# Kernel optimization log

Hardware: AMD Instinct MI355X
Metric: run time of the kernel (lower is better)

The kernel has to match this reference:

```python
import jax, jax.numpy as jnp
import numpy as np

L, B, E, H = 2048, 2, 1024, 16
HD = E // H


def setup_inputs() -> dict:
    key = jax.random.key(0)
    ks = jax.random.split(key, 5)
    s = 0.02
    return {
        "query": jax.random.normal(ks[0], (L, B, E), jnp.float32),
        "key": jax.random.normal(ks[1], (L, B, E), jnp.float32),
        "value": jax.random.normal(ks[2], (L, B, E), jnp.float32),
        "in_proj_weight": jax.random.normal(ks[3], (3 * E, E), jnp.float32) * s,
        "in_proj_bias": jnp.zeros((3 * E,), jnp.float32),
        "out_proj_weight": jax.random.normal(ks[4], (E, E), jnp.float32) * s,
        "out_proj_bias": jnp.zeros((E,), jnp.float32),
    }


def reference(query, key, value, in_proj_weight, in_proj_bias, out_proj_weight, out_proj_bias):
    # torch nn.MultiheadAttention math, seq-first [L, B, E], causal mask
    # (attend_mode='only_attend_front': positions j > i are masked).
    w_q, w_k, w_v = jnp.split(in_proj_weight, 3, axis=0)
    b_q, b_k, b_v = jnpp_split(in_proj_bias) if False else jnp.split(in_proj_bias, 3, axis=0)
    q = query @ w_q.T + b_q            # [L, B, E]
    k = key @ w_k.T + b_k
    v = value @ w_v.T + b_v

    def heads(x):  # [L, B, E] -> [B, H, L, HD]
        return x.reshape(x.shape[0], x.shape[1], H, HD).transpose(1, 2, 0, 3)

    qh, kh, vh = heads(q), heads(k), heads(v)
    scale = 1.0 / jnp.sqrt(jnp.asarray(HD, q.dtype))
    scores = jnp.einsum("bhqd,bhkd->bhqk", qh * scale, kh)  # [B, H, L, L]
    causal = jnp.triu(jnp.ones((scores.shape[-2], scores.shape[-1]), bool), k=1)
    scores = jnp.where(causal, jnp.asarray(-jnp.inf, scores.dtype), scores)
    attn = jax.nn.softmax(scores, axis=-1)
    out = jnp.einsum("bhqk,bhkd->bhqd", attn, vh)           # [B, H, L, HD]
    out = out.transpose(2, 0, 1, 3).reshape(query.shape[0], query.shape[1], E)  # [L, B, E]
    out = out @ out_proj_weight.T + out_proj_bias
    # torch also returns head-averaged attn weights [B, L, L]
    attn_avg = attn.mean(axis=1)
    return out, attn_avg
```

## Files before the change

### kernel.cpp

```cpp
#include <hip/hip_runtime.h>

#define L_ 2048
#define B_ 2
#define E_ 1024
#define H_ 16
#define HD_ 64
#define M_ 4096
#define K_ 1024

typedef unsigned short u16;
typedef unsigned int u32;
using short8  = __attribute__((ext_vector_type(8))) short;
using short4v = __attribute__((ext_vector_type(4))) short;
using floatx4 = __attribute__((ext_vector_type(4))) float;

__device__ inline u16 f2b(float f) {
  unsigned u = __float_as_uint(f);
  u += 0x7FFF + ((u >> 16) & 1);
  return (u16)(u >> 16);
}

__device__ inline u32 pack2(float a, float b) {
  u32 ua = __float_as_uint(a) + 0x8000u;
  u32 ub = __float_as_uint(b) + 0x8000u;
  return (ua >> 16) | (ub & 0xFFFF0000u);
}

__device__ inline floatx4 mfma16(short8 a, short8 b, floatx4 c) {
  return __builtin_amdgcn_mfma_f32_16x16x32_bf16(a, b, c, 0, 0, 0);
}

__device__ inline void gload16(const void* g, void* l) {
  __builtin_amdgcn_global_load_lds(
      (const __attribute__((address_space(1))) u32*)g,
      (__attribute__((address_space(3))) u32*)l, 16, 0, 0);
}

__global__ void convk(const float* __restrict__ src, u16* __restrict__ dst, int n4) {
  int i = blockIdx.x * blockDim.x + threadIdx.x;
  if (i < n4) {
    float4 v = ((const float4*)src)[i];
    ushort4 o;
    o.x = f2b(v.x); o.y = f2b(v.y); o.z = f2b(v.z); o.w = f2b(v.w);
    ((ushort4*)dst)[i] = o;
  }
}

template <int MODE>
__global__ __launch_bounds__(256) void gemm128(
    const u16* __restrict__ A, const u16* __restrict__ W, const float* __restrict__ bias,
    u16* __restrict__ qh, u16* __restrict__ kh, u16* __restrict__ vhT,
    float* __restrict__ outp)
{
  __shared__ __align__(16) u16 As[128 * 32];
  __shared__ __align__(16) u16 Bs[128 * 32];
  const int p = (MODE == 0) ? blockIdx.z : 0;
  const u16* Ap = A + (size_t)p * M_ * K_;
  const u16* Wp = W + (size_t)p * E_ * K_;
  const float* bp = bias + p * E_;
  const int row0 = blockIdx.y * 128, col0 = blockIdx.x * 128;
  const int t = threadIdx.x, lane = t & 63, wv = t >> 6;
  const int lanem = lane & 15, quad = lane >> 4;
  const int wm = wv >> 1, wn = wv & 1;

  int f0 = t, f1 = 256 + t;
  int r0s = f0 >> 2, q0s = (f0 & 3) ^ ((r0s >> 1) & 3);
  int r1s = f1 >> 2, q1s = (f1 & 3) ^ ((r1s >> 1) & 3);

  floatx4 acc[4][4];
#pragma unroll
  for (int mi = 0; mi < 4; ++mi)
#pragma unroll
    for (int ni = 0; ni < 4; ++ni) acc[mi][ni] = (floatx4){0.f, 0.f, 0.f, 0.f};

  const int swz = (lanem >> 1) & 3;

  for (int k0 = 0; k0 < K_; k0 += 32) {
    __syncthreads();
    gload16(Ap + (size_t)(row0 + r0s) * K_ + k0 + q0s * 8, (char*)As + wv * 1024);
    gload16(Wp + (size_t)(col0 + r0s) * K_ + k0 + q0s * 8, (char*)Bs + wv * 1024);
    gload16(Ap + (size_t)(row0 + r1s) * K_ + k0 + q1s * 8, (char*)As + 4096 + wv * 1024);
    gload16(Wp + (size_t)(col0 + r1s) * K_ + k0 + q1s * 8, (char*)Bs + 4096 + wv * 1024);
    __syncthreads();
    short8 af[4], bfg[4];
#pragma unroll
    for (int mi = 0; mi < 4; ++mi) {
      int r = wm * 64 + mi * 16 + lanem;
      af[mi] = *(const short8*)((const char*)As + r * 64 + (quad ^ swz) * 16);
    }
#pragma unroll
    for (int ni = 0; ni < 4; ++ni) {
      int r = wn * 64 + ni * 16 + lanem;
      bfg[ni] = *(const short8*)((const char*)Bs + r * 64 + (quad ^ swz) * 16);
    }
#pragma unroll
    for (int mi = 0; mi < 4; ++mi)
#pragma unroll
      for (int ni = 0; ni < 4; ++ni)
        acc[mi][ni] = mfma16(af[mi], bfg[ni], acc[mi][ni]);
  }

#pragma unroll
  for (int ni = 0; ni < 4; ++ni) {
    int gc = col0 + wn * 64 + ni * 16 + lanem;
    float bv = bp[gc];
#pragma unroll
    for (int mi = 0; mi < 4; ++mi) {
      int gr0 = row0 + wm * 64 + mi * 16 + quad * 4;
#pragma unroll
      for (int v = 0; v < 4; ++v) {
        float val = acc[mi][ni][v] + bv;
        int r = gr0 + v;
        if (MODE == 1) {
          outp[(size_t)r * E_ + gc] = val;
        } else {
          int l = r >> 1, bb = r & 1, hh = gc >> 6, d = gc & 63;
          u16 x = f2b(val);
          if (p == 0)      qh[(((size_t)bb * H_ + hh) * L_ + l) * HD_ + d] = x;
          else if (p == 1) kh[(((size_t)bb * H_ + hh) * L_ + l) * HD_ + d] = x;
          else {
            int lp = (l & ~31) | (((l >> 2) & 3) * 8 + ((l >> 4) & 1) * 4 + (l & 3));
            vhT[(((size_t)bb * H_ + hh) * HD_ + d) * L_ + lp] = x;
          }
        }
      }
    }
  }
}

__global__ __launch_bounds__(256, 4) void attn1(
    const u16* __restrict__ qh, const u16* __restrict__ kh, const u16* __restrict__ vhT,
    u16* __restrict__ ctx, float* __restrict__ li_ws)
{
  __shared__ __align__(16) u16 Ks[64 * 64];
  __shared__ __align__(16) u16 Vs[64 * 64];
  const int it = (L_ / 128 - 1) - blockIdx.x;
  const int h = blockIdx.y, b = blockIdx.z;
  const int t = threadIdx.x, lane = t & 63, wv = t >> 6;
  const int lanem = lane & 15, quad = lane >> 4;
  const int bh = b * H_ + h;
  const int i0 = it * 128;
  const int baseA = i0 + wv * 16;
  const int baseB = i0 + 64 + wv * 16;
  const int rowA = baseA + lanem, rowB = baseB + lanem;

  const u16* qpA = qh + ((size_t)bh * L_ + rowA) * HD_;
  const u16* qpB = qh + ((size_t)bh * L_ + rowB) * HD_;
  short8 qA0 = *(const short8*)(qpA + quad * 8);
  short8 qA1 = *(const short8*)(qpA + 32 + quad * 8);
  short8 qB0 = *(const short8*)(qpB + quad * 8);
  short8 qB1 = *(const short8*)(qpB + 32 + quad * 8);

  const int srow = lane >> 3;
  const int spiece = (lane & 7) ^ srow;
  const u16* ksrc = kh + ((size_t)bh * L_ + wv * 16 + srow) * HD_ + spiece * 8;
  const u16* vsrc = vhT + ((size_t)bh * HD_ + wv * 16 + srow) * L_ + spiece * 8;
  char* kdst = (char*)Ks + wv * 2048;
  char* vdst = (char*)Vs + wv * 2048;

  const int swz = lanem & 7;
  const int cb0 = lanem * 128 + ((quad ^ swz)) * 16;
  const int cb1 = lanem * 128 + ((quad ^ swz) ^ 4) * 16;

  float liA = 0.f, liB = 0.f;
  floatx4 oA[4], oB[4];
#pragma unroll
  for (int d = 0; d < 4; ++d) { oA[d] = (floatx4){0.f,0.f,0.f,0.f}; oB[d] = oA[d]; }

  int j0 = 0;

  auto do_tile = [&](int modeA, int modeB) {
    __syncthreads();
    gload16(ksrc, kdst);
    gload16(ksrc + 8 * HD_, kdst + 1024);
    gload16(vsrc, vdst);
    gload16(vsrc + (size_t)8 * L_, vdst + 1024);
    ksrc += 64 * HD_;
    vsrc += 64;
    __syncthreads();

    floatx4 sA[4], sB[4];
#pragma unroll
    for (int jf = 0; jf < 4; ++jf) {
      short8 a0 = *(const short8*)((const char*)Ks + cb0 + jf * 2048);
      short8 a1 = *(const short8*)((const char*)Ks + cb1 + jf * 2048);
      floatx4 z = (floatx4){0.f,0.f,0.f,0.f};
      if (modeA != 2) sA[jf] = mfma16(a1, qA1, mfma16(a0, qA0, z));
      sB[jf] = mfma16(a1, qB1, mfma16(a0, qB0, z));
    }

    short8 pbA[2], pbB[2];
    auto soft = [&](floatx4* st, int row, float& li, short8* pb, int masked) {
#pragma unroll
      for (int jc = 0; jc < 2; ++jc) {
        float p[8];
#pragma unroll
        for (int r = 0; r < 4; ++r) {
          int ja = j0 + jc * 32 + quad * 4 + r;
          float e0 = __expf(st[jc * 2][r] * 0.125f);
          float e1 = __expf(st[jc * 2 + 1][r] * 0.125f);
          if (masked) {
            e0 = (ja <= row) ? e0 : 0.f;
            e1 = (ja + 16 <= row) ? e1 : 0.f;
          }
          li += e0 + e1;
          p[r] = e0; p[4 + r] = e1;
        }
        union { u32 w[4]; short8 s; } u;
        u.w[0] = pack2(p[0], p[1]); u.w[1] = pack2(p[2], p[3]);
        u.w[2] = pack2(p[4], p[5]); u.w[3] = pack2(p[6], p[7]);
        pb[jc] = u.s;
      }
    };
    if (modeA == 0) soft(sA, rowA, liA, pbA, 0);
    else if (modeA == 1) soft(sA, rowA, liA, pbA, 1);
    if (modeB == 0) soft(sB, rowB, liB, pbB, 0);
    else soft(sB, rowB, liB, pbB, 1);

#pragma unroll
    for (int jc = 0; jc < 2; ++jc) {
      const int base = (jc == 0) ? cb0 : cb1;
#pragma unroll
      for (int dbl = 0; dbl < 4; ++dbl) {
        short8 vf = *(const short8*)((const char*)Vs + base + dbl * 2048);
        if (modeA != 2) oA[dbl] = mfma16(vf, pbA[jc], oA[dbl]);
        oB[dbl] = mfma16(vf, pbB[jc], oB[dbl]);
      }
    }
    j0 += 64;
  };

  for (int jt = 0; jt < 2 * it; ++jt) do_tile(0, 0);
  do_tile(1, 0);
  do_tile(2, 1);

  liA += __shfl_xor(liA, 16); liA += __shfl_xor(liA, 32);
  liB += __shfl_xor(liB, 16); liB += __shfl_xor(liB, 32);
  float invA = 1.0f / liA, invB = 1.0f / liB;

  u16* cA = ctx + ((size_t)rowA * B_ + b) * E_ + h * HD_ + quad * 4;
  u16* cB = ctx + ((size_t)rowB * B_ + b) * E_ + h * HD_ + quad * 4;
#pragma unroll
  for (int dbl = 0; dbl < 4; ++dbl) {
    ushort4 pkA, pkB;
    pkA.x = f2b(oA[dbl][0] * invA); pkA.y = f2b(oA[dbl][1] * invA);
    pkA.z = f2b(oA[dbl][2] * invA); pkA.w = f2b(oA[dbl][3] * invA);
    pkB.x = f2b(oB[dbl][0] * invB); pkB.y = f2b(oB[dbl][1] * invB);
    pkB.z = f2b(oB[dbl][2] * invB); pkB.w = f2b(oB[dbl][3] * invB);
    *(ushort4*)(cA + dbl * 16) = pkA;
    *(ushort4*)(cB + dbl * 16) = pkB;
  }
  if (quad == 0) {
    li_ws[(size_t)bh * L_ + rowA] = invA;
    li_ws[(size_t)bh * L_ + rowB] = invB;
  }
}

__global__ __launch_bounds__(256) void attn2(
    const u16* __restrict__ qh, const u16* __restrict__ kh,
    const float* __restrict__ li_ws, float* __restrict__ out2)
{
  __shared__ __align__(16) u16 Ks[2][2][64 * 64];
  const int jt = blockIdx.x, it = blockIdx.y, b = blockIdx.z;
  const int t = threadIdx.x, lane = t & 63, wv = t >> 6;
  const int lanem = lane & 15, quad = lane >> 4;
  const int i0 = it * 64 + wv * 16;
  const int j0 = jt * 64;
  float* ob = out2 + (size_t)b * L_ * L_;

  if (jt > it) {
    float4 z = {0.f, 0.f, 0.f, 0.f};
    float* rp = ob + (size_t)(i0 + lanem) * L_ + j0 + quad * 16;
    ((float4*)rp)[0] = z; ((float4*)rp)[1] = z;
    ((float4*)rp)[2] = z; ((float4*)rp)[3] = z;
    return;
  }

  const int srow = lane >> 3;
  const int spiece = (lane & 7) ^ srow;
  const int swz = lanem & 7;

  auto stage = [&](int p, int buf) {
#pragma unroll
    for (int hh = 0; hh < 2; ++hh) {
      const u16* kg = kh + ((size_t)(b * H_ + 2 * p + hh) * L_ + j0) * HD_;
#pragma unroll
      for (int k = wv * 2; k < wv * 2 + 2; ++k)
        gload16(kg + (size_t)(k * 8 + srow) * HD_ + spiece * 8,
                (char*)Ks[buf][hh] + k * 1024);
    }
  };
  auto loadQ = [&](int p, short8 q[2][2], floatx4 lf[2]) {
#pragma unroll
    for (int hh = 0; hh < 2; ++hh) {
      int bh = b * H_ + 2 * p + hh;
      const u16* qb = qh + ((size_t)bh * L_ + i0 + lanem) * HD_;
      q[hh][0] = *(const short8*)(qb + quad * 8);
      q[hh][1] = *(const short8*)(qb + 32 + quad * 8);
      lf[hh] = *(const floatx4*)(li_ws + (size_t)bh * L_ + i0 + quad * 4);
    }
  };

  float acc[4][4] = {};
  short8 qc[2][2]; floatx4 lc[2];
  stage(0, 0);
  loadQ(0, qc, lc);

#pragma unroll
  for (int p = 0; p < 8; ++p) {
    const int buf = p & 1;
    if (p < 7) stage(p + 1, 1 - buf);
    __syncthreads();
    short8 qn[2][2]; floatx4 ln[2];
    loadQ(p < 7 ? p + 1 : 7, qn, ln);
#pragma unroll
    for (int hh = 0; hh < 2; ++hh) {
      const char* tb = (const char*)Ks[buf][hh];
#pragma unroll
      for (int s = 0; s < 4; ++s) {
        if (j0 + s * 16 > i0 + 15) continue;
        const char* kr = tb + (s * 16 + lanem) * 128;
        short8 b0 = *(const short8*)(kr + (quad ^ swz) * 16);
        short8 b1 = *(const short8*)(kr + ((4 + quad) ^ swz) * 16);
        floatx4 sv = (floatx4){0.f, 0.f, 0.f, 0.f};
        sv = mfma16(qc[hh][0], b0, sv);
        sv = mfma16(qc[hh][1], b1, sv);
        if (j0 + s * 16 + 15 <= i0) {
#pragma unroll
          for (int r = 0; r < 4; ++r)
            acc[s][r] += __expf(sv[r] * 0.125f) * lc[hh][r];
        } else {
#pragma unroll
          for (int r = 0; r < 4; ++r) {
            int irow = i0 + quad * 4 + r;
            int jc = j0 + s * 16 + lanem;
            if (jc <= irow) acc[s][r] += __expf(sv[r] * 0.125f) * lc[hh][r];
          }
        }
      }
    }
#pragma unroll
    for (int hh = 0; hh < 2; ++hh) {
      qc[hh][0] = qn[hh][0]; qc[hh][1] = qn[hh][1]; lc[hh] = ln[hh];
    }
  }

#pragma unroll
  for (int s = 0; s < 4; ++s)
#pragma unroll
    for (int r = 0; r < 4; ++r) {
      int irow = i0 + quad * 4 + r;
      int jc = j0 + s * 16 + lanem;
      ob[(size_t)irow * L_ + jc] = acc[s][r] * (1.0f / H_);
    }
}

extern "C" void kernel_launch(void* const* d_in, const int* in_sizes, int n_in,
                              void* d_out, int out_size, void* d_ws, size_t ws_size,
                              hipStream_t stream) {
  const float* query = (const float*)d_in[0];
  const float* key   = (const float*)d_in[1];
  const float* value = (const float*)d_in[2];
  const float* w_in  = (const float*)d_in[3];
  const float* b_in  = (const float*)d_in[4];
  const float* w_out = (const float*)d_in[5];
  const float* b_out = (const float*)d_in[6];

  char* ws = (char*)d_ws;
  size_t off = 0;
  auto alloc = [&](size_t bytes) -> void* {
    void* p = ws + off;
    off += (bytes + 255) & ~(size_t)255;
    return p;
  };
  u16* w_in_b  = (u16*)alloc((size_t)3 * E_ * K_ * 2);
  u16* w_out_b = (u16*)alloc((size_t)E_ * K_ * 2);
  u16* x_b     = (u16*)alloc((size_t)3 * M_ * K_ * 2);
  u16* qh      = (u16*)alloc((size_t)B_ * H_ * L_ * HD_ * 2);
  u16* kh      = (u16*)alloc((size_t)B_ * H_ * L_ * HD_ * 2);
  u16* vhT     = (u16*)alloc((size_t)B_ * H_ * L_ * HD_ * 2);
  u16* ctx     = (u16*)alloc((size_t)M_ * E_ * 2);
  float* li_ws = (float*)alloc((size_t)B_ * H_ * L_ * 4);

  convk<<<4096, 256, 0, stream>>>(query, x_b + (size_t)0 * M_ * K_, M_ * K_ / 4);
  convk<<<4096, 256, 0, stream>>>(key,   x_b + (size_t)1 * M_ * K_, M_ * K_ / 4);
  convk<<<4096, 256, 0, stream>>>(value, x_b + (size_t)2 * M_ * K_, M_ * K_ / 4);
  convk<<<3072, 256, 0, stream>>>(w_in,  w_in_b,  3 * E_ * K_ / 4);
  convk<<<1024, 256, 0, stream>>>(w_out, w_out_b, E_ * K_ / 4);

  gemm128<0><<<dim3(E_ / 128, M_ / 128, 3), 256, 0, stream>>>(
      x_b, w_in_b, b_in, qh, kh, vhT, nullptr);

  attn1<<<dim3(L_ / 128, H_, B_), 256, 0, stream>>>(qh, kh, vhT, ctx, li_ws);

  attn2<<<dim3(L_ / 64, L_ / 64, B_), 256, 0, stream>>>(
      qh, kh, li_ws, (float*)d_out + (size_t)M_ * E_);

  gemm128<1><<<dim3(E_ / 128, M_ / 128, 1), 256, 0, stream>>>(
      ctx, w_out_b, b_out, nullptr, nullptr, nullptr, (float*)d_out);
}
```

Before: 286.6 us.

## Double-buffer K/V tiles and pair mirrored row blocks in attention

The causal attention kernel now keeps two shared-memory buffers for K and V. It prefetches the next 64-key tile while computing on the current one, which removes the second barrier that used to wait for each load. Each block now takes one 64-row query block from the front and its mirror from the back, so work per block is more even across the causal triangle. This replaces the earlier pairing of adjacent 128-row halves. The trade-off is twice the LDS per block and launch bounds lowered to 2, which reduces possible occupancy.

```diff
diff --git a/kernel.cpp b/kernel.cpp
--- a/kernel.cpp
+++ b/kernel.cpp
@@ -128,21 +128,20 @@
   }
 }
 
-__global__ __launch_bounds__(256, 4) void attn1(
+__global__ __launch_bounds__(256, 2) void attn1(
     const u16* __restrict__ qh, const u16* __restrict__ kh, const u16* __restrict__ vhT,
     u16* __restrict__ ctx, float* __restrict__ li_ws)
 {
-  __shared__ __align__(16) u16 Ks[64 * 64];
-  __shared__ __align__(16) u16 Vs[64 * 64];
-  const int it = (L_ / 128 - 1) - blockIdx.x;
+  __shared__ __align__(16) u16 Ks[2][64 * 64];
+  __shared__ __align__(16) u16 Vs[2][64 * 64];
+  const int g = blockIdx.x;
   const int h = blockIdx.y, b = blockIdx.z;
   const int t = threadIdx.x, lane = t & 63, wv = t >> 6;
   const int lanem = lane & 15, quad = lane >> 4;
   const int bh = b * H_ + h;
-  const int i0 = it * 128;
-  const int baseA = i0 + wv * 16;
-  const int baseB = i0 + 64 + wv * 16;
-  const int rowA = baseA + lanem, rowB = baseB + lanem;
+  const int gB = (L_ / 64 - 1) - g;
+  const int rowA = g * 64 + wv * 16 + lanem;
+  const int rowB = gB * 64 + wv * 16 + lanem;
 
   const u16* qpA = qh + ((size_t)bh * L_ + rowA) * HD_;
   const u16* qpB = qh + ((size_t)bh * L_ + rowB) * HD_;
@@ -155,8 +154,16 @@
   const int spiece = (lane & 7) ^ srow;
   const u16* ksrc = kh + ((size_t)bh * L_ + wv * 16 + srow) * HD_ + spiece * 8;
   const u16* vsrc = vhT + ((size_t)bh * HD_ + wv * 16 + srow) * L_ + spiece * 8;
-  char* kdst = (char*)Ks + wv * 2048;
-  char* vdst = (char*)Vs + wv * 2048;
+
+  const int ntiles = 32 - g;
+  auto stage = [&](int buf) {
+    gload16(ksrc, (char*)Ks[buf] + wv * 2048);
+    gload16(ksrc + 8 * HD_, (char*)Ks[buf] + wv * 2048 + 1024);
+    gload16(vsrc, (char*)Vs[buf] + wv * 2048);
+    gload16(vsrc + (size_t)8 * L_, (char*)Vs[buf] + wv * 2048 + 1024);
+    ksrc += 64 * HD_;
+    vsrc += 64;
+  };
 
   const int swz = lanem & 7;
   const int cb0 = lanem * 128 + ((quad ^ swz)) * 16;
@@ -167,23 +174,19 @@
 #pragma unroll
   for (int d = 0; d < 4; ++d) { oA[d] = (floatx4){0.f,0.f,0.f,0.f}; oB[d] = oA[d]; }
 
-  int j0 = 0;
+  int j0 = 0, tcur = 0;
 
   auto do_tile = [&](int modeA, int modeB) {
     __syncthreads();
-    gload16(ksrc, kdst);
-    gload16(ksrc + 8 * HD_, kdst + 1024);
-    gload16(vsrc, vdst);
-    gload16(vsrc + (size_t)8 * L_, vdst + 1024);
-    ksrc += 64 * HD_;
-    vsrc += 64;
-    __syncthreads();
+    if (tcur + 1 < ntiles) stage((tcur + 1) & 1);
+    const char* kbuf = (const char*)Ks[tcur & 1];
+    const char* vbuf = (const char*)Vs[tcur & 1];
 
     floatx4 sA[4], sB[4];
 #pragma unroll
     for (int jf = 0; jf < 4; ++jf) {
-      short8 a0 = *(const short8*)((const char*)Ks + cb0 + jf * 2048);
-      short8 a1 = *(const short8*)((const char*)Ks + cb1 + jf * 2048);
+      short8 a0 = *(const short8*)(kbuf + cb0 + jf * 2048);
+      short8 a1 = *(const short8*)(kbuf + cb1 + jf * 2048);
       floatx4 z = (floatx4){0.f,0.f,0.f,0.f};
       if (modeA != 2) sA[jf] = mfma16(a1, qA1, mfma16(a0, qA0, z));
       sB[jf] = mfma16(a1, qB1, mfma16(a0, qB0, z));
@@ -222,16 +225,19 @@
       const int base = (jc == 0) ? cb0 : cb1;
 #pragma unroll
       for (int dbl = 0; dbl < 4; ++dbl) {
-        short8 vf = *(const short8*)((const char*)Vs + base + dbl * 2048);
+        short8 vf = *(const short8*)(vbuf + base + dbl * 2048);
         if (modeA != 2) oA[dbl] = mfma16(vf, pbA[jc], oA[dbl]);
         oB[dbl] = mfma16(vf, pbB[jc], oB[dbl]);
       }
     }
     j0 += 64;
+    ++tcur;
   };
 
-  for (int jt = 0; jt < 2 * it; ++jt) do_tile(0, 0);
+  stage(0);
+  for (int jt = 0; jt < g; ++jt) do_tile(0, 0);
   do_tile(1, 0);
+  for (int jt = g + 1; jt <= 30 - g; ++jt) do_tile(2, 0);
   do_tile(2, 1);
 
   liA += __shfl_xor(liA, 16); liA += __shfl_xor(liA, 32);
```

Measured after the change: 270.1 us. 5.7% less time.
